# Performance work log

Hardware: AMD Instinct MI355X
Metric: run time of the kernel (lower is better)

The kernel has to match this reference:

```python
import jax, jax.numpy as jnp
import numpy as np

N, NN, NI, ND, NH = 20000, 32, 128, 128, 8
RADIUS = 1.0
EPS = 1e-5


def _mlp(x, W1, b1, W2, b2):
    return jax.nn.elu(x @ W1 + b1) @ W2 + b2


def setup_inputs() -> dict:
    key = jax.random.key(0)
    ks = jax.random.split(key, 32)
    s = 0.05
    inp = {
        "features": jax.random.normal(ks[0], (N, NI), jnp.float32),
        "x": jax.random.normal(ks[1], (N, 3), jnp.float32),
        "nuv": jax.random.normal(ks[2], (N, 3, 3), jnp.float32),
        "topk": jax.random.randint(ks[3], (N, NN), 0, N, jnp.int64),
        # query_f: Ni -> Nd -> Nh*Nd
        "qW1": jax.random.normal(ks[4], (NI, ND), jnp.float32) * s,
        "qb1": jnp.zeros((ND,), jnp.float32),
        "qW2": jax.random.normal(ks[5], (ND, NH * ND), jnp.float32) * s,
        "qb2": jnp.zeros((NH * ND,), jnp.float32),
        # geo_encoder: 12 -> Nd -> Nd
        "gW1": jax.random.normal(ks[6], (12, ND), jnp.float32) * s,
        "gb1": jnp.zeros((ND,), jnp.float32),
        "gW2": jax.random.normal(ks[7], (ND, ND), jnp.float32) * s,
        "gb2": jnp.zeros((ND,), jnp.float32),
        # key_f / value_f: Nd -> Nd -> Nd
        "kW1": jax.random.normal(ks[8], (ND, ND), jnp.float32) * s,
        "kb1": jnp.zeros((ND,), jnp.float32),
        "kW2": jax.random.normal(ks[9], (ND, ND), jnp.float32) * s,
        "kb2": jnp.zeros((ND,), jnp.float32),
        "vW1": jax.random.normal(ks[10], (ND, ND), jnp.float32) * s,
        "vb1": jnp.zeros((ND,), jnp.float32),
        "vW2": jax.random.normal(ks[11], (ND, ND), jnp.float32) * s,
        "vb2": jnp.zeros((ND,), jnp.float32),
        # decode_f: Nh*Nd -> Nd -> Nd
        "dW1": jax.random.normal(ks[12], (NH * ND, ND), jnp.float32) * s,
        "db1": jnp.zeros((ND,), jnp.float32),
        "dW2": jax.random.normal(ks[13], (ND, ND), jnp.float32) * s,
        "db2": jnp.zeros((ND,), jnp.float32),
        # LayerNorm
        "ln_g": jnp.ones((ND,), jnp.float32),
        "ln_b": jnp.zeros((ND,), jnp.float32),
    }
    return inp


def reference(features, x, nuv, topk, qW1, qb1, qW2, qb2, gW1, gb1, gW2, gb2,
              kW1, kb1, kW2, kb2, vW1, vb1, vW2, vb2, dW1, db1, dW2, db2,
              ln_g, ln_b):
    n, nn = topk.shape
    sdk = jnp.sqrt(jnp.float32(ND))

    Q = _mlp(features, qW1, qb1, qW2, qb2).reshape(n, NH, ND)  # (N,Nh,Nd)

    features_nn = features[topk]              # (N,nn,Nd)
    x_nn = x[topk]                            # (N,nn,3)
    orient_x = x_nn - x[:, None, :]           # (N,nn,3)
    nuv_nn = nuv[topk].reshape(n, nn * 3, 3)  # (N,nn*3,3)

    dis2 = jnp.sum(orient_x * orient_x, axis=2, keepdims=True)
    dis = jnp.exp(-dis2 / (2.0 * RADIUS * RADIUS))  # (N,nn,1)

    # rotate neighbor offsets / frames into local frame: nuv @ v^T, then transpose
    RL_x = jnp.einsum('nij,nkj->nki', nuv, orient_x)            # (N,nn,3)
    RL_nuv = jnp.einsum('nij,nkj->nki', nuv, nuv_nn)            # (N,nn*3,3)
    RL_nuv = RL_nuv.reshape(n, nn, 9)
    RL = jnp.concatenate([RL_x, RL_nuv], axis=-1)               # (N,nn,12)

    geo_fea = _mlp(RL, gW1, gb1, gW2, gb2)
    geo_fea = dis * geo_fea * features_nn                       # (N,nn,Nd)

    K = _mlp(geo_fea, kW1, kb1, kW2, kb2)                       # (N,nn,Nd)
    V = _mlp(geo_fea, vW1, vb1, vW2, vb2)                       # (N,nn,Nd)

    Mq = jnp.einsum('nhd,nkd->nhk', Q, K)                       # (N,Nh,nn)
    mask = (topk == 0)[:, None, :]                              # (N,1,nn)
    Mq = jnp.where(mask, -jnp.inf, Mq)
    Mq = jax.nn.softmax(Mq / sdk, axis=2)

    out = jnp.einsum('nhk,nkd->nhd', Mq, V).reshape(n, NH * ND)
    out = _mlp(out, dW1, db1, dW2, db2) + features

    mu = jnp.mean(out, axis=-1, keepdims=True)
    var = jnp.var(out, axis=-1, keepdims=True)
    return (out - mu) / jnp.sqrt(var + EPS) * ln_g + ln_b
```

## Files before the change

### kernel.cpp

```cpp
#include <hip/hip_runtime.h>
#include <math.h>
#include <stdint.h>

#define ND 128
#define NNB 32
#define NH 8

typedef __attribute__((ext_vector_type(8))) short bf16x8;
typedef __attribute__((ext_vector_type(4))) float f32x4;
typedef __attribute__((ext_vector_type(8))) unsigned short u16x8;
typedef __attribute__((ext_vector_type(2))) unsigned int u32x2;
typedef unsigned short u16;
typedef unsigned int u32;
typedef unsigned long long u64;

#define OFF_QW1T 0ULL
#define OFF_QW2T 32768ULL
#define OFF_GW1T 294912ULL
#define OFF_GW2T 303104ULL
#define OFF_KW1T 335872ULL
#define OFF_KW2T 368640ULL
#define OFF_VW1T 401408ULL
#define OFF_VW2T 434176ULL
#define OFF_DW1T 466944ULL
#define OFF_DW2T 729088ULL
#define OFF_Q    761856ULL
#define OFF_ATT  (OFF_Q + 20096ULL * 2048ULL)

#define SBAR() asm volatile("s_waitcnt lgkmcnt(0)\n\ts_barrier" ::: "memory")

__device__ __forceinline__ u16 rneb(float f){
    u32 u = __builtin_bit_cast(u32, f);
    u32 r = u + 0x7fffu + ((u >> 16) & 1u);
    return (u16)(r >> 16);
}
__device__ __forceinline__ float elu_f(float v){ return v > 0.f ? v : (__expf(v) - 1.f); }

__device__ __forceinline__ u32 cvtpk(float a, float b){
    u32 r;
    asm("v_cvt_pk_bf16_f32 %0, %1, %2" : "=v"(r) : "v"(a), "v"(b));
    return r;
}
__device__ __forceinline__ u32x2 cvt4(float a, float b, float c, float d){
    u32x2 r; r.x = cvtpk(a, b); r.y = cvtpk(c, d); return r;
}

#define GLDS16(g, l) __builtin_amdgcn_global_load_lds( \
    (const __attribute__((address_space(1))) u32*)(g), \
    (__attribute__((address_space(3))) u32*)(u32)(u64)(l), 16, 0, 0)

__device__ __forceinline__ bf16x8 ldfrag(const u16* base, int row, int kb, int l){
    int r = row + (l & 15);
    int byte = (r << 8) + (((kb << 1) + ((l >> 4) << 4)) ^ ((r & 7) << 4));
    return *(const bf16x8*)((const char*)base + byte);
}
__device__ __forceinline__ bf16x8 ldfragRL(const u16* base, int row, int l){
    int r = row + (l & 15);
    int byte = (r << 6) + ((((l >> 4) << 4)) ^ ((r & 3) << 4));
    return *(const bf16x8*)((const char*)base + byte);
}
__device__ __forceinline__ bf16x8 ldfragG(const char* __restrict__ Wt, int n, int kstride, int kb, int l){
    return *(const bf16x8*)(Wt + (size_t)(n + (l & 15)) * (size_t)kstride
                               + (size_t)((kb << 1) + ((l >> 4) << 4)));
}

__device__ __forceinline__ void gemm_half(const bf16x8 aw[4][2], const u16* B,
                                          int nbase, f32x4 acc[2][4], int l){
    __builtin_amdgcn_s_setprio(1);
    #pragma unroll
    for (int kk = 0; kk < 4; kk++){
        #pragma unroll
        for (int nt = 0; nt < 4; nt++){
            bf16x8 b = ldfrag(B, nbase + nt * 16, kk * 32, l);
            acc[0][nt] = __builtin_amdgcn_mfma_f32_16x16x32_bf16(aw[kk][0], b, acc[0][nt], 0, 0, 0);
            acc[1][nt] = __builtin_amdgcn_mfma_f32_16x16x32_bf16(aw[kk][1], b, acc[1][nt], 0, 0, 0);
        }
    }
    __builtin_amdgcn_s_setprio(0);
}

__device__ __forceinline__ void bias_init2(f32x4 acc[2][4], const float* __restrict__ bias,
                                           int m0, int hi){
    #pragma unroll
    for (int mt = 0; mt < 2; mt++){
        float4 bq = *(const float4*)&bias[m0 + mt * 16 + (hi << 2)];
        #pragma unroll
        for (int nt = 0; nt < 4; nt++)
            acc[mt][nt] = (f32x4){bq.x, bq.y, bq.z, bq.w};
    }
}

template<int ACT, bool INPLACE>
__device__ __forceinline__ void layerP(
    const u16* inB, u16* outB, const bf16x8 aw[4][2],
    const float* __restrict__ bias, const float* __restrict__ F,
    const int* sidx, const float* sdis, int m0, int l, int hi)
{
    #pragma unroll
    for (int half = 0; half < 2; half++){
        const int nbase = half * 64;
        float4 fv[2][4]; float ds[4];
        if (ACT == 2){
            #pragma unroll
            for (int nt = 0; nt < 4; nt++){
                int row = nbase + nt * 16 + (l & 15);
                int ix = sidx[row];
                ds[nt] = sdis[row];
                fv[0][nt] = *(const float4*)&F[(size_t)ix * ND + m0 + (hi << 2)];
                fv[1][nt] = *(const float4*)&F[(size_t)ix * ND + m0 + 16 + (hi << 2)];
            }
        }
        f32x4 acc[2][4];
        bias_init2(acc, bias, m0, hi);
        gemm_half(aw, inB, nbase, acc, l);
        if (INPLACE) SBAR();
        #pragma unroll
        for (int mt = 0; mt < 2; mt++){
            int ch0 = m0 + mt * 16 + (hi << 2);
            #pragma unroll
            for (int nt = 0; nt < 4; nt++){
                int row = nbase + nt * 16 + (l & 15);
                float v0 = acc[mt][nt][0], v1 = acc[mt][nt][1];
                float v2 = acc[mt][nt][2], v3 = acc[mt][nt][3];
                if (ACT == 1){ v0 = elu_f(v0); v1 = elu_f(v1); v2 = elu_f(v2); v3 = elu_f(v3); }
                if (ACT == 2){
                    float s = ds[nt];
                    v0 *= s * fv[mt][nt].x; v1 *= s * fv[mt][nt].y;
                    v2 *= s * fv[mt][nt].z; v3 *= s * fv[mt][nt].w;
                }
                *(u32x2*)((char*)outB + (row << 8) + (((ch0 << 1)) ^ ((row & 7) << 4))) =
                    cvt4(v0, v1, v2, v3);
            }
        }
    }
    SBAR();
}

struct PrepDesc {
    const float* src[10];
    u64 dstoff[10];
    int N[10], Ksrc[10], Kdst[10];
};

__global__ __launch_bounds__(256) void prep_weights(PrepDesc d, char* ws){
    int tid = blockIdx.x * 256 + threadIdx.x;
    #pragma unroll 1
    for (int m = 0; m < 10; m++){
        int cnt = (d.Kdst[m] * d.N[m]) >> 3;
        if (tid < cnt){
            int N = d.N[m];
            int nn = tid % N, k8 = tid / N;
            const float* s = d.src[m];
            u16x8 pk;
            #pragma unroll
            for (int i = 0; i < 8; i++){
                int k = k8 * 8 + i;
                pk[i] = (k < d.Ksrc[m]) ? rneb(s[(size_t)k * N + nn]) : (u16)0;
            }
            *(u16x8*)(ws + d.dstoff[m] + (u64)nn * (u64)(d.Kdst[m] * 2) + (u64)(k8 * 16)) = pk;
            return;
        }
        tid -= cnt;
    }
}

__device__ __forceinline__ void gemm2x4G(const char* __restrict__ Wt, int kstride, int kbase,
                                         const u16* B, f32x4 acc[2][4], int m0, int n0, int l){
    bf16x8 aw[4][2];
    #pragma unroll
    for (int kk = 0; kk < 4; kk++)
        #pragma unroll
        for (int i = 0; i < 2; i++)
            aw[kk][i] = ldfragG(Wt, m0 + i * 16, kstride, kbase + kk * 32, l);
    __builtin_amdgcn_s_setprio(1);
    #pragma unroll
    for (int kk = 0; kk < 4; kk++){
        #pragma unroll
        for (int nt = 0; nt < 4; nt++){
            bf16x8 b = ldfrag(B, n0 + nt * 16, kk * 32, l);
            #pragma unroll
            for (int mt = 0; mt < 2; mt++)
                acc[mt][nt] = __builtin_amdgcn_mfma_f32_16x16x32_bf16(aw[kk][mt], b, acc[mt][nt], 0, 0, 0);
        }
    }
    __builtin_amdgcn_s_setprio(0);
}

__global__ __launch_bounds__(512, 2) void qmlp_kernel(
    const float* __restrict__ F, const float* __restrict__ qb1, const float* __restrict__ qb2,
    const char* __restrict__ ws, u16* __restrict__ Qg, int n)
{
    __shared__ __align__(16) u16 sIn[16384];
    __shared__ __align__(16) u16 sH[16384];
    const int t = threadIdx.x;
    const int row0 = blockIdx.x * 128;
    const int l = t & 63, w = t >> 6;
    const int m0 = (w & 3) * 32, n0 = (w >> 2) * 64;
    const int hi = l >> 4;

    for (int i = t; i < 4096; i += 512){
        int r = i >> 5, c = (i & 31) * 4;
        int gr = row0 + r;
        float4 v = make_float4(0.f, 0.f, 0.f, 0.f);
        if (gr < n) v = *(const float4*)&F[(size_t)gr * ND + c];
        *(u32x2*)((char*)sIn + (r << 8) + (((c << 1)) ^ ((r & 7) << 4))) = cvt4(v.x, v.y, v.z, v.w);
    }
    SBAR();

    {
        f32x4 acc[2][4];
        bias_init2(acc, qb1, m0, hi);
        gemm2x4G(ws + OFF_QW1T, 256, 0, sIn, acc, m0, n0, l);
        #pragma unroll
        for (int mt = 0; mt < 2; mt++){
            int ch0 = m0 + mt * 16 + (hi << 2);
            #pragma unroll
            for (int nt = 0; nt < 4; nt++){
                int row = n0 + nt * 16 + (l & 15);
                *(u32x2*)((char*)sH + (row << 8) + (((ch0 << 1)) ^ ((row & 7) << 4))) =
                    cvt4(elu_f(acc[mt][nt][0]), elu_f(acc[mt][nt][1]),
                         elu_f(acc[mt][nt][2]), elu_f(acc[mt][nt][3]));
            }
        }
    }
    SBAR();

    for (int ct = 0; ct < 8; ct++){
        f32x4 a2[2][4];
        bias_init2(a2, qb2 + ct * 128, m0, hi);
        gemm2x4G(ws + OFF_QW2T + (u64)ct * 32768ULL, 256, 0, sH, a2, m0, n0, l);
        #pragma unroll
        for (int mt = 0; mt < 2; mt++){
            int ch0 = m0 + mt * 16 + (hi << 2);
            #pragma unroll
            for (int nt = 0; nt < 4; nt++){
                int row = n0 + nt * 16 + (l & 15);
                int gr = row0 + row;
                if (gr < n)
                    *(u64*)((char*)Qg + (size_t)gr * 2048 + (size_t)((ct * 128 + ch0) * 2)) =
                        __builtin_bit_cast(u64, cvt4(a2[mt][nt][0], a2[mt][nt][1],
                                                     a2[mt][nt][2], a2[mt][nt][3]));
            }
        }
    }
}

__global__ __launch_bounds__(256, 2) void attn_kernel(
    const float* __restrict__ F, const float* __restrict__ X,
    const float* __restrict__ NUV, const int* __restrict__ TOPK,
    const float* __restrict__ gb1, const float* __restrict__ gb2,
    const float* __restrict__ kb1, const float* __restrict__ kb2,
    const float* __restrict__ vb1, const float* __restrict__ vb2,
    const char* __restrict__ ws, const u16* __restrict__ Qg, u16* __restrict__ ATT,
    int ngroups)
{
    __shared__ __align__(16) u16 bufA[16384];
    __shared__ __align__(16) u16 bufB[16384];
    __shared__ __align__(16) u16 sP16[2048];
    __shared__ float sdis[128];
    __shared__ int   sidx[128];

    const int t = threadIdx.x;
    const int l = t & 63, w = t >> 6;
    const int m0 = w * 32;
    const int hi = l >> 4;

    bf16x8 ag[2];
    #pragma unroll
    for (int i = 0; i < 2; i++)
        ag[i] = *(const bf16x8*)(ws + OFF_GW1T
                 + (u64)((m0 + i * 16 + (l & 15)) * 64 + (hi << 4)));
    bf16x8 wg2[4][2], wk1[4][2], wk2[4][2], wv1[4][2], wv2[4][2];
    #pragma unroll
    for (int kk = 0; kk < 4; kk++)
        #pragma unroll
        for (int i = 0; i < 2; i++){
            u64 fo = (u64)((m0 + i * 16 + (l & 15)) * 256 + kk * 64 + (hi << 4));
            wg2[kk][i] = *(const bf16x8*)(ws + OFF_GW2T + fo);
            wk1[kk][i] = *(const bf16x8*)(ws + OFF_KW1T + fo);
            wk2[kk][i] = *(const bf16x8*)(ws + OFF_KW2T + fo);
            wv1[kk][i] = *(const bf16x8*)(ws + OFF_VW1T + fo);
            wv2[kk][i] = *(const bf16x8*)(ws + OFF_VW2T + fo);
        }

    for (int g = blockIdx.x; g < ngroups; g += gridDim.x){
        const int pid0 = g * 4;
        SBAR();

        if (t < 128){
            int p = t >> 5, k = t & 31;
            int pid = pid0 + p;
            int idx = TOPK[(size_t)pid * NNB + k];
            sidx[t] = idx;
            float x0 = X[(size_t)pid * 3 + 0], x1 = X[(size_t)pid * 3 + 1], x2 = X[(size_t)pid * 3 + 2];
            float ox = X[(size_t)idx * 3 + 0] - x0;
            float oy = X[(size_t)idx * 3 + 1] - x1;
            float oz = X[(size_t)idx * 3 + 2] - x2;
            sdis[t] = __expf(-0.5f * (ox * ox + oy * oy + oz * oz));
            float nv[9];
            #pragma unroll
            for (int i = 0; i < 9; i++) nv[i] = NUV[(size_t)pid * 9 + i];
            float f[12];
            #pragma unroll
            for (int i = 0; i < 3; i++)
                f[i] = nv[i * 3 + 0] * ox + nv[i * 3 + 1] * oy + nv[i * 3 + 2] * oz;
            #pragma unroll
            for (int r = 0; r < 3; r++){
                float a0 = NUV[(size_t)idx * 9 + r * 3 + 0];
                float a1 = NUV[(size_t)idx * 9 + r * 3 + 1];
                float a2 = NUV[(size_t)idx * 9 + r * 3 + 2];
                #pragma unroll
                for (int i = 0; i < 3; i++)
                    f[3 + r * 3 + i] = nv[i * 3 + 0] * a0 + nv[i * 3 + 1] * a1 + nv[i * 3 + 2] * a2;
            }
            char* rb = (char*)bufB + (t << 6);
            u32 key = (u32)(t & 3) << 4;
            *(u32x2*)(rb + (0u ^ key))  = cvt4(f[0], f[1], f[2], f[3]);
            *(u32x2*)(rb + (8u ^ key))  = cvt4(f[4], f[5], f[6], f[7]);
            *(u32x2*)(rb + (16u ^ key)) = cvt4(f[8], f[9], f[10], f[11]);
            *(u32x2*)(rb + (24u ^ key)) = (u32x2){0u, 0u};
            *(u32x2*)(rb + (32u ^ key)) = (u32x2){0u, 0u};
            *(u32x2*)(rb + (40u ^ key)) = (u32x2){0u, 0u};
            *(u32x2*)(rb + (48u ^ key)) = (u32x2){0u, 0u};
            *(u32x2*)(rb + (56u ^ key)) = (u32x2){0u, 0u};
        }
        SBAR();

        #pragma unroll
        for (int half = 0; half < 2; half++){
            f32x4 acc[2][4];
            bias_init2(acc, gb1, m0, hi);
            __builtin_amdgcn_s_setprio(1);
            #pragma unroll
            for (int nt = 0; nt < 4; nt++){
                bf16x8 bg = ldfragRL(bufB, half * 64 + nt * 16, l);
                acc[0][nt] = __builtin_amdgcn_mfma_f32_16x16x32_bf16(ag[0], bg, acc[0][nt], 0, 0, 0);
                acc[1][nt] = __builtin_amdgcn_mfma_f32_16x16x32_bf16(ag[1], bg, acc[1][nt], 0, 0, 0);
            }
            __builtin_amdgcn_s_setprio(0);
            #pragma unroll
            for (int mt = 0; mt < 2; mt++){
                int ch0 = m0 + mt * 16 + (hi << 2);
                #pragma unroll
                for (int nt = 0; nt < 4; nt++){
                    int row = half * 64 + nt * 16 + (l & 15);
                    *(u32x2*)((char*)bufA + (row << 8) + (((ch0 << 1)) ^ ((row & 7) << 4))) =
                        cvt4(elu_f(acc[mt][nt][0]), elu_f(acc[mt][nt][1]),
                             elu_f(acc[mt][nt][2]), elu_f(acc[mt][nt][3]));
                }
            }
        }
        SBAR();

        layerP<2, false>(bufA, bufB, wg2, gb2, F, sidx, sdis, m0, l, hi);
        layerP<1, false>(bufB, bufA, wk1, kb1, F, sidx, sdis, m0, l, hi);
        layerP<0, true >(bufA, bufA, wk2, kb2, F, sidx, sdis, m0, l, hi);

        {
            f32x4 s0, s1;
            s0 = 0.f; s1 = 0.f;
            const char* qb = (const char*)Qg + (size_t)(pid0 + w) * 2048
                           + (size_t)(l & 7) * 256 + (size_t)(hi << 4);
            #pragma unroll
            for (int kk = 0; kk < 4; kk++){
                bf16x8 bq = *(const bf16x8*)(qb + kk * 64);
                bf16x8 a0 = ldfrag(bufA, w * 32,      kk * 32, l);
                bf16x8 a1 = ldfrag(bufA, w * 32 + 16, kk * 32, l);
                s0 = __builtin_amdgcn_mfma_f32_16x16x32_bf16(a0, bq, s0, 0, 0, 0);
                s1 = __builtin_amdgcn_mfma_f32_16x16x32_bf16(a1, bq, s1, 0, 0, 0);
            }
            const float RS = 0.08838834764831845f;
            float sv[8];
            #pragma unroll
            for (int mt = 0; mt < 2; mt++)
                #pragma unroll
                for (int j = 0; j < 4; j++){
                    int kidx = mt * 16 + (hi << 2) + j;
                    float x = (mt ? s1[j] : s0[j]) * RS;
                    if (sidx[w * 32 + kidx] == 0) x = -INFINITY;
                    sv[mt * 4 + j] = x;
                }
            float mx = sv[0];
            #pragma unroll
            for (int i = 1; i < 8; i++) mx = fmaxf(mx, sv[i]);
            mx = fmaxf(mx, __shfl_xor(mx, 16));
            mx = fmaxf(mx, __shfl_xor(mx, 32));
            float e[8], sum = 0.f;
            #pragma unroll
            for (int i = 0; i < 8; i++){ e[i] = __expf(sv[i] - mx); sum += e[i]; }
            sum += __shfl_xor(sum, 16);
            sum += __shfl_xor(sum, 32);
            float inv = 1.f / sum;
            int h = l & 15;
            u32 key = (u32)(h & 3) << 4;
            char* pb = (char*)sP16 + w * 1024 + h * 64;
            *(u32x2*)(pb + (((u32)(hi * 8)) ^ key)) =
                cvt4(e[0] * inv, e[1] * inv, e[2] * inv, e[3] * inv);
            *(u32x2*)(pb + (((u32)(32 + hi * 8)) ^ key)) =
                cvt4(e[4] * inv, e[5] * inv, e[6] * inv, e[7] * inv);
        }
        SBAR();

        layerP<1, false>(bufB, bufA, wv1, vb1, F, sidx, sdis, m0, l, hi);

        #pragma unroll
        for (int half = 0; half < 2; half++){
            f32x4 a2[4][2];
            #pragma unroll
            for (int ntc = 0; ntc < 2; ntc++){
                float bv = vb2[m0 + ntc * 16 + (l & 15)];
                #pragma unroll
                for (int mtr = 0; mtr < 4; mtr++)
                    a2[mtr][ntc] = (f32x4){bv, bv, bv, bv};
            }
            __builtin_amdgcn_s_setprio(1);
            #pragma unroll
            for (int kk = 0; kk < 4; kk++){
                #pragma unroll
                for (int mtr = 0; mtr < 4; mtr++){
                    bf16x8 a = ldfrag(bufA, half * 64 + mtr * 16, kk * 32, l);
                    #pragma unroll
                    for (int ntc = 0; ntc < 2; ntc++)
                        a2[mtr][ntc] = __builtin_amdgcn_mfma_f32_16x16x32_bf16(a, wv2[kk][ntc], a2[mtr][ntc], 0, 0, 0);
                }
            }
            __builtin_amdgcn_s_setprio(0);
            #pragma unroll
            for (int mtr = 0; mtr < 4; mtr++){
                int kv0 = half * 64 + mtr * 16 + (hi << 2);
                #pragma unroll
                for (int ntc = 0; ntc < 2; ntc++){
                    int ch = m0 + ntc * 16 + (l & 15);
                    *(u32x2*)((char*)bufB + (ch << 8) + (((kv0 << 1)) ^ ((ch & 7) << 4))) =
                        cvt4(a2[mtr][ntc][0], a2[mtr][ntc][1], a2[mtr][ntc][2], a2[mtr][ntc][3]);
                }
            }
        }
        SBAR();

        {
            int pid = pid0 + w;
            int h = l & 15;
            bf16x8 pb = *(const bf16x8*)((const char*)sP16 + w * 1024 + h * 64
                                         + (((u32)(hi * 16)) ^ ((u32)(h & 3) << 4)));
            u32 key = ((u32)pid & 7) << 4;
            char* dst = (char*)ATT + (size_t)pid * 2048;
            #pragma unroll
            for (int nt = 0; nt < 8; nt++){
                f32x4 o;
                o = 0.f;
                bf16x8 av = ldfrag(bufB, nt * 16, w * 32, l);
                o = __builtin_amdgcn_mfma_f32_16x16x32_bf16(av, pb, o, 0, 0, 0);
                if (h < 8){
                    u32 dbyte = (u32)(nt * 32 + hi * 8);
                    *(u32x2*)(dst + h * 256 + (dbyte ^ key)) = cvt4(o[0], o[1], o[2], o[3]);
                }
            }
        }
    }
}

__global__ __launch_bounds__(512, 2) void decode_kernel(
    const u16* __restrict__ ATT,
    const float* __restrict__ db1, const float* __restrict__ db2,
    const float* __restrict__ F,
    const float* __restrict__ lng, const float* __restrict__ lnb,
    const char* __restrict__ ws, float* __restrict__ OUT, int n)
{
    __shared__ __align__(16) char SM[67584];
    u16* sA = (u16*)SM;
    u16* sH = (u16*)(SM + 32768);
    float* sO = (float*)SM;

    const int t = threadIdx.x;
    const int row0 = blockIdx.x * 128;
    const int l = t & 63, w = t >> 6;
    const int m0 = (w & 3) * 32, n0 = (w >> 2) * 64;
    const int hi = l >> 4;

    f32x4 acc[2][4];
    bias_init2(acc, db1, m0, hi);
    for (int kc = 0; kc < 8; kc++){
        {
            const int seg = (t & 15) * 16, rr = t >> 4;
            const char* g = (const char*)ATT + (size_t)row0 * 2048 + kc * 256;
            #pragma unroll
            for (int i = 0; i < 4; i++){
                int row = i * 32 + rr;
                GLDS16(g + (size_t)row * 2048 + seg, (char*)sA + row * 256 + seg);
            }
        }
        __syncthreads();
        gemm2x4G(ws + OFF_DW1T, 2048, kc * 128, sA, acc, m0, n0, l);
        SBAR();
    }
    #pragma unroll
    for (int mt = 0; mt < 2; mt++){
        int ch0 = m0 + mt * 16 + (hi << 2);
        #pragma unroll
        for (int nt = 0; nt < 4; nt++){
            int row = n0 + nt * 16 + (l & 15);
            *(u32x2*)((char*)sH + (row << 8) + (((ch0 << 1)) ^ ((row & 7) << 4))) =
                cvt4(elu_f(acc[mt][nt][0]), elu_f(acc[mt][nt][1]),
                     elu_f(acc[mt][nt][2]), elu_f(acc[mt][nt][3]));
        }
    }
    SBAR();

    f32x4 a2[2][4];
    bias_init2(a2, db2, m0, hi);
    gemm2x4G(ws + OFF_DW2T, 256, 0, sH, a2, m0, n0, l);
    SBAR();

    #pragma unroll
    for (int mt = 0; mt < 2; mt++){
        int ch0 = m0 + mt * 16 + (hi << 2);
        #pragma unroll
        for (int nt = 0; nt < 4; nt++){
            int row = n0 + nt * 16 + (l & 15);
            int gr = row0 + row;
            float4 fres = make_float4(0.f, 0.f, 0.f, 0.f);
            if (gr < n) fres = *(const float4*)&F[(size_t)gr * ND + ch0];
            float4 ov = make_float4(a2[mt][nt][0] + fres.x, a2[mt][nt][1] + fres.y,
                                    a2[mt][nt][2] + fres.z, a2[mt][nt][3] + fres.w);
            *(float4*)&sO[row * 132 + ch0] = ov;
        }
    }
    SBAR();

    {
        int r = t >> 2, q = t & 3;
        const float* rowp = sO + r * 132 + q * 32;
        float s = 0.f;
        #pragma unroll
        for (int i = 0; i < 8; i++){
            float4 v = ((const float4*)rowp)[i];
            s += v.x + v.y + v.z + v.w;
        }
        s += __shfl_xor(s, 1);
        s += __shfl_xor(s, 2);
        float mu = s * (1.0f / 128.0f);
        float q2 = 0.f;
        #pragma unroll
        for (int i = 0; i < 8; i++){
            float4 v = ((const float4*)rowp)[i];
            q2 += (v.x - mu) * (v.x - mu) + (v.y - mu) * (v.y - mu)
                + (v.z - mu) * (v.z - mu) + (v.w - mu) * (v.w - mu);
        }
        q2 += __shfl_xor(q2, 1);
        q2 += __shfl_xor(q2, 2);
        float rstd = rsqrtf(q2 * (1.0f / 128.0f) + 1e-5f);
        int gr = row0 + r;
        if (gr < n){
            #pragma unroll
            for (int i = 0; i < 8; i++){
                float4 v = ((const float4*)rowp)[i];
                int c = q * 32 + i * 4;
                float4 g4 = *(const float4*)&lng[c];
                float4 b4 = *(const float4*)&lnb[c];
                float4 ov = make_float4((v.x - mu) * rstd * g4.x + b4.x,
                                        (v.y - mu) * rstd * g4.y + b4.y,
                                        (v.z - mu) * rstd * g4.z + b4.z,
                                        (v.w - mu) * rstd * g4.w + b4.w);
                *(float4*)&OUT[(size_t)gr * ND + c] = ov;
            }
        }
    }
}

extern "C" void kernel_launch(void* const* d_in, const int* in_sizes, int n_in,
                              void* d_out, int out_size, void* d_ws, size_t ws_size,
                              hipStream_t stream)
{
    const float* F    = (const float*)d_in[0];
    const float* X    = (const float*)d_in[1];
    const float* NUV  = (const float*)d_in[2];
    const int*   TOPK = (const int*)d_in[3];
    const float* qW1  = (const float*)d_in[4];
    const float* qb1  = (const float*)d_in[5];
    const float* qW2  = (const float*)d_in[6];
    const float* qb2  = (const float*)d_in[7];
    const float* gW1  = (const float*)d_in[8];
    const float* gb1  = (const float*)d_in[9];
    const float* gW2  = (const float*)d_in[10];
    const float* gb2  = (const float*)d_in[11];
    const float* kW1  = (const float*)d_in[12];
    const float* kb1  = (const float*)d_in[13];
    const float* kW2  = (const float*)d_in[14];
    const float* kb2  = (const float*)d_in[15];
    const float* vW1  = (const float*)d_in[16];
    const float* vb1  = (const float*)d_in[17];
    const float* vW2  = (const float*)d_in[18];
    const float* vb2  = (const float*)d_in[19];
    const float* dW1  = (const float*)d_in[20];
    const float* db1  = (const float*)d_in[21];
    const float* dW2  = (const float*)d_in[22];
    const float* db2  = (const float*)d_in[23];
    const float* lng  = (const float*)d_in[24];
    const float* lnb  = (const float*)d_in[25];

    const int n = in_sizes[0] / ND;
    char* wsb = (char*)d_ws;

    PrepDesc pd;
    const float* srcs[10] = {qW1, qW2, gW1, gW2, kW1, kW2, vW1, vW2, dW1, dW2};
    u64 offs[10] = {OFF_QW1T, OFF_QW2T, OFF_GW1T, OFF_GW2T, OFF_KW1T,
                    OFF_KW2T, OFF_VW1T, OFF_VW2T, OFF_DW1T, OFF_DW2T};
    int Ns[10]   = {128, 1024, 128, 128, 128, 128, 128, 128, 128, 128};
    int Ksrc[10] = {128, 128, 12, 128, 128, 128, 128, 128, 1024, 128};
    int Kdst[10] = {128, 128, 32, 128, 128, 128, 128, 128, 1024, 128};
    for (int i = 0; i < 10; i++){
        pd.src[i] = srcs[i]; pd.dstoff[i] = offs[i];
        pd.N[i] = Ns[i]; pd.Ksrc[i] = Ksrc[i]; pd.Kdst[i] = Kdst[i];
    }
    prep_weights<<<186, 256, 0, stream>>>(pd, wsb);

    u16* Qg  = (u16*)(wsb + OFF_Q);
    u16* ATT = (u16*)(wsb + OFF_ATT);
    const int nb = (n + 127) / 128;
    const int ngroups = n / 4;

    qmlp_kernel<<<nb, 512, 0, stream>>>(F, qb1, qb2, wsb, Qg, n);
    attn_kernel<<<512, 256, 0, stream>>>(F, X, NUV, TOPK, gb1, gb2,
                                         kb1, kb2, vb1, vb2, wsb, Qg, ATT, ngroups);
    decode_kernel<<<nb, 512, 0, stream>>>(ATT, db1, db2, F, lng, lnb, wsb, (float*)d_out, n);
}
```

Measured before the change: 393.3 us.

## Make attention per-wave independent with global weight fragments and bf16 feature copy

New measurement: 530.2 us. 1.35x slower.

```diff
diff --git a/kernel.cpp b/kernel.cpp
--- a/kernel.cpp
+++ b/kernel.cpp
@@ -26,14 +26,22 @@
 #define OFF_DW2T 729088ULL
 #define OFF_Q    761856ULL
 #define OFF_ATT  (OFF_Q + 20096ULL * 2048ULL)
+#define OFF_FB   (OFF_ATT + 20096ULL * 2048ULL)
+#define WS_NEED  (OFF_FB + 20096ULL * 256ULL)
 
 #define SBAR() asm volatile("s_waitcnt lgkmcnt(0)\n\ts_barrier" ::: "memory")
+
+__device__ __forceinline__ void waveFence(){
+    asm volatile("s_waitcnt lgkmcnt(0)" ::: "memory");
+    __builtin_amdgcn_sched_barrier(0);
+}
 
 __device__ __forceinline__ u16 rneb(float f){
     u32 u = __builtin_bit_cast(u32, f);
     u32 r = u + 0x7fffu + ((u >> 16) & 1u);
     return (u16)(r >> 16);
 }
+__device__ __forceinline__ float b2f(u16 h){ return __builtin_bit_cast(float, (u32)h << 16); }
 __device__ __forceinline__ float elu_f(float v){ return v > 0.f ? v : (__expf(v) - 1.f); }
 
 __device__ __forceinline__ u32 cvtpk(float a, float b){
@@ -64,76 +72,83 @@
                                + (size_t)((kb << 1) + ((l >> 4) << 4)));
 }
 
-__device__ __forceinline__ void gemm_half(const bf16x8 aw[4][2], const u16* B,
-                                          int nbase, f32x4 acc[2][4], int l){
+template<int ACT>
+__device__ __forceinline__ void layerV(
+    const u16* inT, u16* outT, const char* __restrict__ Wt,
+    const float* __restrict__ bias,
+    const u16* __restrict__ Fb, const float* __restrict__ F,
+    const int* six, const float* sds, int l, int hi)
+{
+    const int ln = l & 15;
+    bf16x8 b[2][4];
+    #pragma unroll
+    for (int nt = 0; nt < 2; nt++)
+        #pragma unroll
+        for (int kk = 0; kk < 4; kk++)
+            b[nt][kk] = ldfrag(inT, nt * 16, kk * 32, l);
+    f32x4 acc[8][2];
+    #pragma unroll
+    for (int mt = 0; mt < 8; mt++){
+        float4 bq = *(const float4*)&bias[mt * 16 + (hi << 2)];
+        acc[mt][0] = (f32x4){bq.x, bq.y, bq.z, bq.w};
+        acc[mt][1] = acc[mt][0];
+    }
     __builtin_amdgcn_s_setprio(1);
     #pragma unroll
     for (int kk = 0; kk < 4; kk++){
         #pragma unroll
-        for (int nt = 0; nt < 4; nt++){
-            bf16x8 b = ldfrag(B, nbase + nt * 16, kk * 32, l);
-            acc[0][nt] = __builtin_amdgcn_mfma_f32_16x16x32_bf16(aw[kk][0], b, acc[0][nt], 0, 0, 0);
-            acc[1][nt] = __builtin_amdgcn_mfma_f32_16x16x32_bf16(aw[kk][1], b, acc[1][nt], 0, 0, 0);
+        for (int mt = 0; mt < 8; mt++){
+            bf16x8 aw = ldfragG(Wt, mt * 16, 256, kk * 32, l);
+            acc[mt][0] = __builtin_amdgcn_mfma_f32_16x16x32_bf16(aw, b[0][kk], acc[mt][0], 0, 0, 0);
+            acc[mt][1] = __builtin_amdgcn_mfma_f32_16x16x32_bf16(aw, b[1][kk], acc[mt][1], 0, 0, 0);
         }
     }
     __builtin_amdgcn_s_setprio(0);
-}
-
-__device__ __forceinline__ void bias_init2(f32x4 acc[2][4], const float* __restrict__ bias,
-                                           int m0, int hi){
-    #pragma unroll
-    for (int mt = 0; mt < 2; mt++){
-        float4 bq = *(const float4*)&bias[m0 + mt * 16 + (hi << 2)];
-        #pragma unroll
-        for (int nt = 0; nt < 4; nt++)
-            acc[mt][nt] = (f32x4){bq.x, bq.y, bq.z, bq.w};
-    }
-}
-
-template<int ACT, bool INPLACE>
-__device__ __forceinline__ void layerP(
-    const u16* inB, u16* outB, const bf16x8 aw[4][2],
-    const float* __restrict__ bias, const float* __restrict__ F,
-    const int* sidx, const float* sdis, int m0, int l, int hi)
-{
-    #pragma unroll
-    for (int half = 0; half < 2; half++){
-        const int nbase = half * 64;
-        float4 fv[2][4]; float ds[4];
-        if (ACT == 2){
-            #pragma unroll
-            for (int nt = 0; nt < 4; nt++){
-                int row = nbase + nt * 16 + (l & 15);
-                int ix = sidx[row];
-                ds[nt] = sdis[row];
-                fv[0][nt] = *(const float4*)&F[(size_t)ix * ND + m0 + (hi << 2)];
-                fv[1][nt] = *(const float4*)&F[(size_t)ix * ND + m0 + 16 + (hi << 2)];
-            }
-        }
-        f32x4 acc[2][4];
-        bias_init2(acc, bias, m0, hi);
-        gemm_half(aw, inB, nbase, acc, l);
-        if (INPLACE) SBAR();
-        #pragma unroll
-        for (int mt = 0; mt < 2; mt++){
-            int ch0 = m0 + mt * 16 + (hi << 2);
-            #pragma unroll
-            for (int nt = 0; nt < 4; nt++){
-                int row = nbase + nt * 16 + (l & 15);
-                float v0 = acc[mt][nt][0], v1 = acc[mt][nt][1];
-                float v2 = acc[mt][nt][2], v3 = acc[mt][nt][3];
-                if (ACT == 1){ v0 = elu_f(v0); v1 = elu_f(v1); v2 = elu_f(v2); v3 = elu_f(v3); }
-                if (ACT == 2){
-                    float s = ds[nt];
-                    v0 *= s * fv[mt][nt].x; v1 *= s * fv[mt][nt].y;
-                    v2 *= s * fv[mt][nt].z; v3 *= s * fv[mt][nt].w;
+    u32x2 gb[8][2]; float4 gf[8][2]; float ds[2];
+    if (ACT == 2){
+        #pragma unroll
+        for (int nt = 0; nt < 2; nt++){
+            int row = nt * 16 + ln;
+            int ix = six[row];
+            ds[nt] = sds[row];
+            if (Fb){
+                #pragma unroll
+                for (int mt = 0; mt < 8; mt++)
+                    gb[mt][nt] = *(const u32x2*)&Fb[(size_t)ix * ND + mt * 16 + (hi << 2)];
+            } else {
+                #pragma unroll
+                for (int mt = 0; mt < 8; mt++)
+                    gf[mt][nt] = *(const float4*)&F[(size_t)ix * ND + mt * 16 + (hi << 2)];
+            }
+        }
+    }
+    waveFence();
+    #pragma unroll
+    for (int mt = 0; mt < 8; mt++){
+        int ch0 = mt * 16 + (hi << 2);
+        #pragma unroll
+        for (int nt = 0; nt < 2; nt++){
+            int row = nt * 16 + ln;
+            float v0 = acc[mt][nt][0], v1 = acc[mt][nt][1];
+            float v2 = acc[mt][nt][2], v3 = acc[mt][nt][3];
+            if (ACT == 1){ v0 = elu_f(v0); v1 = elu_f(v1); v2 = elu_f(v2); v3 = elu_f(v3); }
+            if (ACT == 2){
+                float s = ds[nt];
+                if (Fb){
+                    v0 *= s * b2f((u16)(gb[mt][nt].x & 0xffffu));
+                    v1 *= s * b2f((u16)(gb[mt][nt].x >> 16));
+                    v2 *= s * b2f((u16)(gb[mt][nt].y & 0xffffu));
+                    v3 *= s * b2f((u16)(gb[mt][nt].y >> 16));
+                } else {
+                    v0 *= s * gf[mt][nt].x; v1 *= s * gf[mt][nt].y;
+                    v2 *= s * gf[mt][nt].z; v3 *= s * gf[mt][nt].w;
                 }
-                *(u32x2*)((char*)outB + (row << 8) + (((ch0 << 1)) ^ ((row & 7) << 4))) =
-                    cvt4(v0, v1, v2, v3);
-            }
-        }
-    }
-    SBAR();
+            }
+            *(u32x2*)((char*)outT + (row << 8) + (((ch0 << 1)) ^ ((row & 7) << 4))) =
+                cvt4(v0, v1, v2, v3);
+        }
+    }
+    waveFence();
 }
 
 struct PrepDesc {
@@ -164,6 +179,17 @@
     }
 }
 
+__device__ __forceinline__ void bias_init2(f32x4 acc[2][4], const float* __restrict__ bias,
+                                           int m0, int hi){
+    #pragma unroll
+    for (int mt = 0; mt < 2; mt++){
+        float4 bq = *(const float4*)&bias[m0 + mt * 16 + (hi << 2)];
+        #pragma unroll
+        for (int nt = 0; nt < 4; nt++)
+            acc[mt][nt] = (f32x4){bq.x, bq.y, bq.z, bq.w};
+    }
+}
+
 __device__ __forceinline__ void gemm2x4G(const char* __restrict__ Wt, int kstride, int kbase,
                                          const u16* B, f32x4 acc[2][4], int m0, int n0, int l){
     bf16x8 aw[4][2];
@@ -188,7 +214,7 @@
 
 __global__ __launch_bounds__(512, 2) void qmlp_kernel(
     const float* __restrict__ F, const float* __restrict__ qb1, const float* __restrict__ qb2,
-    const char* __restrict__ ws, u16* __restrict__ Qg, int n)
+    const char* __restrict__ ws, u16* __restrict__ Qg, u16* __restrict__ Fb, int n)
 {
     __shared__ __align__(16) u16 sIn[16384];
     __shared__ __align__(16) u16 sH[16384];
@@ -203,7 +229,9 @@
         int gr = row0 + r;
         float4 v = make_float4(0.f, 0.f, 0.f, 0.f);
         if (gr < n) v = *(const float4*)&F[(size_t)gr * ND + c];
-        *(u32x2*)((char*)sIn + (r << 8) + (((c << 1)) ^ ((r & 7) << 4))) = cvt4(v.x, v.y, v.z, v.w);
+        u32x2 pk = cvt4(v.x, v.y, v.z, v.w);
+        *(u32x2*)((char*)sIn + (r << 8) + (((c << 1)) ^ ((r & 7) << 4))) = pk;
+        if (Fb && gr < n) *(u32x2*)&Fb[(size_t)gr * ND + c] = pk;
     }
     SBAR();
 
@@ -251,210 +279,203 @@
     const float* __restrict__ gb1, const float* __restrict__ gb2,
     const float* __restrict__ kb1, const float* __restrict__ kb2,
     const float* __restrict__ vb1, const float* __restrict__ vb2,
-    const char* __restrict__ ws, const u16* __restrict__ Qg, u16* __restrict__ ATT,
-    int ngroups)
+    const char* __restrict__ ws, const u16* __restrict__ Qg,
+    const u16* __restrict__ Fb, u16* __restrict__ ATT)
 {
-    __shared__ __align__(16) u16 bufA[16384];
-    __shared__ __align__(16) u16 bufB[16384];
+    __shared__ __align__(16) u16 bufX[16384];
+    __shared__ __align__(16) u16 bufY[16384];
     __shared__ __align__(16) u16 sP16[2048];
     __shared__ float sdis[128];
     __shared__ int   sidx[128];
 
     const int t = threadIdx.x;
     const int l = t & 63, w = t >> 6;
-    const int m0 = w * 32;
-    const int hi = l >> 4;
-
-    bf16x8 ag[2];
-    #pragma unroll
-    for (int i = 0; i < 2; i++)
-        ag[i] = *(const bf16x8*)(ws + OFF_GW1T
-                 + (u64)((m0 + i * 16 + (l & 15)) * 64 + (hi << 4)));
-    bf16x8 wg2[4][2], wk1[4][2], wk2[4][2], wv1[4][2], wv2[4][2];
-    #pragma unroll
-    for (int kk = 0; kk < 4; kk++)
-        #pragma unroll
-        for (int i = 0; i < 2; i++){
-            u64 fo = (u64)((m0 + i * 16 + (l & 15)) * 256 + kk * 64 + (hi << 4));
-            wg2[kk][i] = *(const bf16x8*)(ws + OFF_GW2T + fo);
-            wk1[kk][i] = *(const bf16x8*)(ws + OFF_KW1T + fo);
-            wk2[kk][i] = *(const bf16x8*)(ws + OFF_KW2T + fo);
-            wv1[kk][i] = *(const bf16x8*)(ws + OFF_VW1T + fo);
-            wv2[kk][i] = *(const bf16x8*)(ws + OFF_VW2T + fo);
-        }
-
-    for (int g = blockIdx.x; g < ngroups; g += gridDim.x){
-        const int pid0 = g * 4;
-        SBAR();
-
-        if (t < 128){
-            int p = t >> 5, k = t & 31;
-            int pid = pid0 + p;
-            int idx = TOPK[(size_t)pid * NNB + k];
-            sidx[t] = idx;
-            float x0 = X[(size_t)pid * 3 + 0], x1 = X[(size_t)pid * 3 + 1], x2 = X[(size_t)pid * 3 + 2];
-            float ox = X[(size_t)idx * 3 + 0] - x0;
-            float oy = X[(size_t)idx * 3 + 1] - x1;
-            float oz = X[(size_t)idx * 3 + 2] - x2;
-            sdis[t] = __expf(-0.5f * (ox * ox + oy * oy + oz * oz));
-            float nv[9];
-            #pragma unroll
-            for (int i = 0; i < 9; i++) nv[i] = NUV[(size_t)pid * 9 + i];
-            float f[12];
+    const int hi = l >> 4, ln = l & 15;
+    const int pid = blockIdx.x * 4 + w;
+
+    u16* bX = bufX + w * 4096;
+    u16* bY = bufY + w * 4096;
+    u16* sPw = sP16 + w * 512;
+    int*   six = sidx + w * 32;
+    float* sds = sdis + w * 32;
+
+    if (l < 32){
+        int k = l;
+        int idx = TOPK[(size_t)pid * NNB + k];
+        six[k] = idx;
+        float x0 = X[(size_t)pid * 3 + 0], x1 = X[(size_t)pid * 3 + 1], x2 = X[(size_t)pid * 3 + 2];
+        float ox = X[(size_t)idx * 3 + 0] - x0;
+        float oy = X[(size_t)idx * 3 + 1] - x1;
+        float oz = X[(size_t)idx * 3 + 2] - x2;
+        sds[k] = __expf(-0.5f * (ox * ox + oy * oy + oz * oz));
+        float nv[9];
+        #pragma unroll
+        for (int i = 0; i < 9; i++) nv[i] = NUV[(size_t)pid * 9 + i];
+        float f[12];
+        #pragma unroll
+        for (int i = 0; i < 3; i++)
+            f[i] = nv[i * 3 + 0] * ox + nv[i * 3 + 1] * oy + nv[i * 3 + 2] * oz;
+        #pragma unroll
+        for (int r = 0; r < 3; r++){
+            float a0 = NUV[(size_t)idx * 9 + r * 3 + 0];
+            float a1 = NUV[(size_t)idx * 9 + r * 3 + 1];
+            float a2 = NUV[(size_t)idx * 9 + r * 3 + 2];
             #pragma unroll
             for (int i = 0; i < 3; i++)
-                f[i] = nv[i * 3 + 0] * ox + nv[i * 3 + 1] * oy + nv[i * 3 + 2] * oz;
-            #pragma unroll
-            for (int r = 0; r < 3; r++){
-                float a0 = NUV[(size_t)idx * 9 + r * 3 + 0];
-                float a1 = NUV[(size_t)idx * 9 + r * 3 + 1];
-                float a2 = NUV[(size_t)idx * 9 + r * 3 + 2];
-                #pragma unroll
-                for (int i = 0; i < 3; i++)
-                    f[3 + r * 3 + i] = nv[i * 3 + 0] * a0 + nv[i * 3 + 1] * a1 + nv[i * 3 + 2] * a2;
-            }
-            char* rb = (char*)bufB + (t << 6);
-            u32 key = (u32)(t & 3) << 4;
-            *(u32x2*)(rb + (0u ^ key))  = cvt4(f[0], f[1], f[2], f[3]);
-            *(u32x2*)(rb + (8u ^ key))  = cvt4(f[4], f[5], f[6], f[7]);
-            *(u32x2*)(rb + (16u ^ key)) = cvt4(f[8], f[9], f[10], f[11]);
-            *(u32x2*)(rb + (24u ^ key)) = (u32x2){0u, 0u};
-            *(u32x2*)(rb + (32u ^ key)) = (u32x2){0u, 0u};
-            *(u32x2*)(rb + (40u ^ key)) = (u32x2){0u, 0u};
-            *(u32x2*)(rb + (48u ^ key)) = (u32x2){0u, 0u};
-            *(u32x2*)(rb + (56u ^ key)) = (u32x2){0u, 0u};
-        }
-        SBAR();
-
-        #pragma unroll
-        for (int half = 0; half < 2; half++){
-            f32x4 acc[2][4];
-            bias_init2(acc, gb1, m0, hi);
-            __builtin_amdgcn_s_setprio(1);
-            #pragma unroll
-            for (int nt = 0; nt < 4; nt++){
-                bf16x8 bg = ldfragRL(bufB, half * 64 + nt * 16, l);
-                acc[0][nt] = __builtin_amdgcn_mfma_f32_16x16x32_bf16(ag[0], bg, acc[0][nt], 0, 0, 0);
-                acc[1][nt] = __builtin_amdgcn_mfma_f32_16x16x32_bf16(ag[1], bg, acc[1][nt], 0, 0, 0);
-            }
-            __builtin_amdgcn_s_setprio(0);
-            #pragma unroll
-            for (int mt = 0; mt < 2; mt++){
-                int ch0 = m0 + mt * 16 + (hi << 2);
-                #pragma unroll
-                for (int nt = 0; nt < 4; nt++){
-                    int row = half * 64 + nt * 16 + (l & 15);
-                    *(u32x2*)((char*)bufA + (row << 8) + (((ch0 << 1)) ^ ((row & 7) << 4))) =
-                        cvt4(elu_f(acc[mt][nt][0]), elu_f(acc[mt][nt][1]),
-                             elu_f(acc[mt][nt][2]), elu_f(acc[mt][nt][3]));
-                }
-            }
-        }
-        SBAR();
-
-        layerP<2, false>(bufA, bufB, wg2, gb2, F, sidx, sdis, m0, l, hi);
-        layerP<1, false>(bufB, bufA, wk1, kb1, F, sidx, sdis, m0, l, hi);
-        layerP<0, true >(bufA, bufA, wk2, kb2, F, sidx, sdis, m0, l, hi);
-
-        {
-            f32x4 s0, s1;
-            s0 = 0.f; s1 = 0.f;
-            const char* qb = (const char*)Qg + (size_t)(pid0 + w) * 2048
-                           + (size_t)(l & 7) * 256 + (size_t)(hi << 4);
-            #pragma unroll
-            for (int kk = 0; kk < 4; kk++){
-                bf16x8 bq = *(const bf16x8*)(qb + kk * 64);
-                bf16x8 a0 = ldfrag(bufA, w * 32,      kk * 32, l);
-                bf16x8 a1 = ldfrag(bufA, w * 32 + 16, kk * 32, l);
-                s0 = __builtin_amdgcn_mfma_f32_16x16x32_bf16(a0, bq, s0, 0, 0, 0);
-                s1 = __builtin_amdgcn_mfma_f32_16x16x32_bf16(a1, bq, s1, 0, 0, 0);
-            }
-            const float RS = 0.08838834764831845f;
-            float sv[8];
-            #pragma unroll
-            for (int mt = 0; mt < 2; mt++)
-                #pragma unroll
-                for (int j = 0; j < 4; j++){
-                    int kidx = mt * 16 + (hi << 2) + j;
-                    float x = (mt ? s1[j] : s0[j]) * RS;
-                    if (sidx[w * 32 + kidx] == 0) x = -INFINITY;
-                    sv[mt * 4 + j] = x;
-                }
-            float mx = sv[0];
-            #pragma unroll
-            for (int i = 1; i < 8; i++) mx = fmaxf(mx, sv[i]);
-            mx = fmaxf(mx, __shfl_xor(mx, 16));
-            mx = fmaxf(mx, __shfl_xor(mx, 32));
-            float e[8], sum = 0.f;
-            #pragma unroll
-            for (int i = 0; i < 8; i++){ e[i] = __expf(sv[i] - mx); sum += e[i]; }
-            sum += __shfl_xor(sum, 16);
-            sum += __shfl_xor(sum, 32);
-            float inv = 1.f / sum;
-            int h = l & 15;
-            u32 key = (u32)(h & 3) << 4;
-            char* pb = (char*)sP16 + w * 1024 + h * 64;
-            *(u32x2*)(pb + (((u32)(hi * 8)) ^ key)) =
-                cvt4(e[0] * inv, e[1] * inv, e[2] * inv, e[3] * inv);
-            *(u32x2*)(pb + (((u32)(32 + hi * 8)) ^ key)) =
-                cvt4(e[4] * inv, e[5] * inv, e[6] * inv, e[7] * inv);
-        }
-        SBAR();
-
-        layerP<1, false>(bufB, bufA, wv1, vb1, F, sidx, sdis, m0, l, hi);
-
-        #pragma unroll
-        for (int half = 0; half < 2; half++){
-            f32x4 a2[4][2];
-            #pragma unroll
-            for (int ntc = 0; ntc < 2; ntc++){
-                float bv = vb2[m0 + ntc * 16 + (l & 15)];
-                #pragma unroll
-                for (int mtr = 0; mtr < 4; mtr++)
-                    a2[mtr][ntc] = (f32x4){bv, bv, bv, bv};
-            }
-            __builtin_amdgcn_s_setprio(1);
-            #pragma unroll
-            for (int kk = 0; kk < 4; kk++){
-                #pragma unroll
-                for (int mtr = 0; mtr < 4; mtr++){
-                    bf16x8 a = ldfrag(bufA, half * 64 + mtr * 16, kk * 32, l);
-                    #pragma unroll
-                    for (int ntc = 0; ntc < 2; ntc++)
-                        a2[mtr][ntc] = __builtin_amdgcn_mfma_f32_16x16x32_bf16(a, wv2[kk][ntc], a2[mtr][ntc], 0, 0, 0);
-                }
-            }
-            __builtin_amdgcn_s_setprio(0);
-            #pragma unroll
-            for (int mtr = 0; mtr < 4; mtr++){
-                int kv0 = half * 64 + mtr * 16 + (hi << 2);
-                #pragma unroll
-                for (int ntc = 0; ntc < 2; ntc++){
-                    int ch = m0 + ntc * 16 + (l & 15);
-                    *(u32x2*)((char*)bufB + (ch << 8) + (((kv0 << 1)) ^ ((ch & 7) << 4))) =
-                        cvt4(a2[mtr][ntc][0], a2[mtr][ntc][1], a2[mtr][ntc][2], a2[mtr][ntc][3]);
-                }
-            }
-        }
-        SBAR();
-
-        {
-            int pid = pid0 + w;
-            int h = l & 15;
-            bf16x8 pb = *(const bf16x8*)((const char*)sP16 + w * 1024 + h * 64
-                                         + (((u32)(hi * 16)) ^ ((u32)(h & 3) << 4)));
-            u32 key = ((u32)pid & 7) << 4;
-            char* dst = (char*)ATT + (size_t)pid * 2048;
-            #pragma unroll
-            for (int nt = 0; nt < 8; nt++){
-                f32x4 o;
-                o = 0.f;
-                bf16x8 av = ldfrag(bufB, nt * 16, w * 32, l);
-                o = __builtin_amdgcn_mfma_f32_16x16x32_bf16(av, pb, o, 0, 0, 0);
-                if (h < 8){
-                    u32 dbyte = (u32)(nt * 32 + hi * 8);
-                    *(u32x2*)(dst + h * 256 + (dbyte ^ key)) = cvt4(o[0], o[1], o[2], o[3]);
-                }
+                f[3 + r * 3 + i] = nv[i * 3 + 0] * a0 + nv[i * 3 + 1] * a1 + nv[i * 3 + 2] * a2;
+        }
+        char* rb = (char*)bY + (k << 6);
+        u32 key = (u32)(k & 3) << 4;
+        *(u32x2*)(rb + (0u ^ key))  = cvt4(f[0], f[1], f[2], f[3]);
+        *(u32x2*)(rb + (8u ^ key))  = cvt4(f[4], f[5], f[6], f[7]);
+        *(u32x2*)(rb + (16u ^ key)) = cvt4(f[8], f[9], f[10], f[11]);
+        *(u32x2*)(rb + (24u ^ key)) = (u32x2){0u, 0u};
+        *(u32x2*)(rb + (32u ^ key)) = (u32x2){0u, 0u};
+        *(u32x2*)(rb + (40u ^ key)) = (u32x2){0u, 0u};
+        *(u32x2*)(rb + (48u ^ key)) = (u32x2){0u, 0u};
+        *(u32x2*)(rb + (56u ^ key)) = (u32x2){0u, 0u};
+    }
+    waveFence();
+
+    {
+        bf16x8 bg[2];
+        #pragma unroll
+        for (int nt = 0; nt < 2; nt++) bg[nt] = ldfragRL(bY, nt * 16, l);
+        f32x4 acc[8][2];
+        #pragma unroll
+        for (int mt = 0; mt < 8; mt++){
+            float4 bq = *(const float4*)&gb1[mt * 16 + (hi << 2)];
+            acc[mt][0] = (f32x4){bq.x, bq.y, bq.z, bq.w};
+            acc[mt][1] = acc[mt][0];
+        }
+        __builtin_amdgcn_s_setprio(1);
+        #pragma unroll
+        for (int mt = 0; mt < 8; mt++){
+            bf16x8 aw = ldfragG(ws + OFF_GW1T, mt * 16, 64, 0, l);
+            acc[mt][0] = __builtin_amdgcn_mfma_f32_16x16x32_bf16(aw, bg[0], acc[mt][0], 0, 0, 0);
+            acc[mt][1] = __builtin_amdgcn_mfma_f32_16x16x32_bf16(aw, bg[1], acc[mt][1], 0, 0, 0);
+        }
+        __builtin_amdgcn_s_setprio(0);
+        waveFence();
+        #pragma unroll
+        for (int mt = 0; mt < 8; mt++){
+            int ch0 = mt * 16 + (hi << 2);
+            #pragma unroll
+            for (int nt = 0; nt < 2; nt++){
+                int row = nt * 16 + ln;
+                *(u32x2*)((char*)bX + (row << 8) + (((ch0 << 1)) ^ ((row & 7) << 4))) =
+                    cvt4(elu_f(acc[mt][nt][0]), elu_f(acc[mt][nt][1]),
+                         elu_f(acc[mt][nt][2]), elu_f(acc[mt][nt][3]));
+            }
+        }
+    }
+    waveFence();
+
+    layerV<2>(bX, bY, ws + OFF_GW2T, gb2, Fb, F, six, sds, l, hi);
+    layerV<1>(bY, bX, ws + OFF_KW1T, kb1, Fb, F, six, sds, l, hi);
+    layerV<0>(bX, bX, ws + OFF_KW2T, kb2, Fb, F, six, sds, l, hi);
+
+    {
+        f32x4 s0, s1;
+        s0 = 0.f; s1 = 0.f;
+        const char* qb = (const char*)Qg + (size_t)pid * 2048
+                       + (size_t)(l & 7) * 256 + (size_t)(hi << 4);
+        #pragma unroll
+        for (int kk = 0; kk < 4; kk++){
+            bf16x8 bq = *(const bf16x8*)(qb + kk * 64);
+            bf16x8 a0 = ldfrag(bX, 0,  kk * 32, l);
+            bf16x8 a1 = ldfrag(bX, 16, kk * 32, l);
+            s0 = __builtin_amdgcn_mfma_f32_16x16x32_bf16(a0, bq, s0, 0, 0, 0);
+            s1 = __builtin_amdgcn_mfma_f32_16x16x32_bf16(a1, bq, s1, 0, 0, 0);
+        }
+        const float RS = 0.08838834764831845f;
+        float sv[8];
+        #pragma unroll
+        for (int mt = 0; mt < 2; mt++)
+            #pragma unroll
+            for (int j = 0; j < 4; j++){
+                int kidx = mt * 16 + (hi << 2) + j;
+                float x = (mt ? s1[j] : s0[j]) * RS;
+                if (six[kidx] == 0) x = -INFINITY;
+                sv[mt * 4 + j] = x;
+            }
+        float mx = sv[0];
+        #pragma unroll
+        for (int i = 1; i < 8; i++) mx = fmaxf(mx, sv[i]);
+        mx = fmaxf(mx, __shfl_xor(mx, 16));
+        mx = fmaxf(mx, __shfl_xor(mx, 32));
+        float e[8], sum = 0.f;
+        #pragma unroll
+        for (int i = 0; i < 8; i++){ e[i] = __expf(sv[i] - mx); sum += e[i]; }
+        sum += __shfl_xor(sum, 16);
+        sum += __shfl_xor(sum, 32);
+        float inv = 1.f / sum;
+        int h = ln;
+        u32 key = (u32)(h & 3) << 4;
+        char* pb = (char*)sPw + h * 64;
+        *(u32x2*)(pb + (((u32)(hi * 8)) ^ key)) =
+            cvt4(e[0] * inv, e[1] * inv, e[2] * inv, e[3] * inv);
+        *(u32x2*)(pb + (((u32)(32 + hi * 8)) ^ key)) =
+            cvt4(e[4] * inv, e[5] * inv, e[6] * inv, e[7] * inv);
+    }
+    waveFence();
+
+    layerV<1>(bY, bX, ws + OFF_VW1T, vb1, Fb, F, six, sds, l, hi);
+
+    {
+        bf16x8 a[2][4];
+        #pragma unroll
+        for (int mtr = 0; mtr < 2; mtr++)
+            #pragma unroll
+            for (int kk = 0; kk < 4; kk++)
+                a[mtr][kk] = ldfrag(bX, mtr * 16, kk * 32, l);
+        f32x4 a2[2][8];
+        #pragma unroll
+        for (int ntc = 0; ntc < 8; ntc++){
+            float bv = vb2[ntc * 16 + ln];
+            a2[0][ntc] = (f32x4){bv, bv, bv, bv};
+            a2[1][ntc] = a2[0][ntc];
+        }
+        __builtin_amdgcn_s_setprio(1);
+        #pragma unroll
+        for (int kk = 0; kk < 4; kk++){
+            #pragma unroll
+            for (int ntc = 0; ntc < 8; ntc++){
+                bf16x8 bw = ldfragG(ws + OFF_VW2T, ntc * 16, 256, kk * 32, l);
+                a2[0][ntc] = __builtin_amdgcn_mfma_f32_16x16x32_bf16(a[0][kk], bw, a2[0][ntc], 0, 0, 0);
+                a2[1][ntc] = __builtin_amdgcn_mfma_f32_16x16x32_bf16(a[1][kk], bw, a2[1][ntc], 0, 0, 0);
+            }
+        }
+        __builtin_amdgcn_s_setprio(0);
+        waveFence();
+        #pragma unroll
+        for (int mtr = 0; mtr < 2; mtr++){
+            int kv0 = mtr * 16 + (hi << 2);
+            #pragma unroll
+            for (int ntc = 0; ntc < 8; ntc++){
+                int ch = ntc * 16 + ln;
+                *(u32x2*)((char*)bY + (ch << 6) + (((u32)(kv0 << 1)) ^ ((u32)(ch & 3) << 4))) =
+                    cvt4(a2[mtr][ntc][0], a2[mtr][ntc][1], a2[mtr][ntc][2], a2[mtr][ntc][3]);
+            }
+        }
+    }
+    waveFence();
+
+    {
+        int h = ln;
+        bf16x8 pb = *(const bf16x8*)((const char*)sPw + h * 64
+                                     + (((u32)(hi * 16)) ^ ((u32)(h & 3) << 4)));
+        u32 key = ((u32)pid & 7) << 4;
+        char* dst = (char*)ATT + (size_t)pid * 2048;
+        #pragma unroll
+        for (int mt = 0; mt < 8; mt++){
+            f32x4 o;
+            o = 0.f;
+            bf16x8 av = ldfragRL(bY, mt * 16, l);
+            o = __builtin_amdgcn_mfma_f32_16x16x32_bf16(av, pb, o, 0, 0, 0);
+            if (h < 8){
+                u32 dbyte = (u32)(mt * 32 + hi * 8);
+                *(u32x2*)(dst + h * 256 + (dbyte ^ key)) = cvt4(o[0], o[1], o[2], o[3]);
             }
         }
     }
@@ -601,6 +622,7 @@
 
     const int n = in_sizes[0] / ND;
     char* wsb = (char*)d_ws;
+    const bool useFb = (ws_size >= (size_t)WS_NEED);
 
     PrepDesc pd;
     const float* srcs[10] = {qW1, qW2, gW1, gW2, kW1, kW2, vW1, vW2, dW1, dW2};
@@ -617,11 +639,11 @@
 
     u16* Qg  = (u16*)(wsb + OFF_Q);
     u16* ATT = (u16*)(wsb + OFF_ATT);
+    u16* Fb  = useFb ? (u16*)(wsb + OFF_FB) : (u16*)nullptr;
     const int nb = (n + 127) / 128;
-    const int ngroups = n / 4;
-
-    qmlp_kernel<<<nb, 512, 0, stream>>>(F, qb1, qb2, wsb, Qg, n);
-    attn_kernel<<<512, 256, 0, stream>>>(F, X, NUV, TOPK, gb1, gb2,
-                                         kb1, kb2, vb1, vb2, wsb, Qg, ATT, ngroups);
+
+    qmlp_kernel<<<nb, 512, 0, stream>>>(F, qb1, qb2, wsb, Qg, Fb, n);
+    attn_kernel<<<n / 4, 256, 0, stream>>>(F, X, NUV, TOPK, gb1, gb2,
+                                           kb1, kb2, vb1, vb2, wsb, Qg, Fb, ATT);
     decode_kernel<<<nb, 512, 0, stream>>>(ATT, db1, db2, F, lng, lnb, wsb, (float*)d_out, n);
 }
```
